# Performance work log

Measured on AMD Instinct MI355X. Metric: run time of the kernel, lower is better.

The kernel has to match this reference:

```python
import jax, jax.numpy as jnp
import numpy as np

N = 50000      # nodes
E = 800000     # directed edges (before self-loops)
FEAT = 120     # raw node feature dim
TOPO = 8       # topological feature dim
H1, D1 = 8, 8  # conv1: heads, per-head dim
C = 40         # out_channels (classes)
NEG_SLOPE = 0.2


def setup_inputs() -> dict:
    key = jax.random.key(0)
    ks = jax.random.split(key, 10)
    return {
        "x": jax.random.normal(ks[0], (N, FEAT), dtype=jnp.float32),
        "topo": jax.random.normal(ks[1], (N, TOPO), dtype=jnp.float32),
        "edge_index": jax.random.randint(ks[2], (2, E), 0, N, dtype=jnp.int32),
        "W1": jax.random.normal(ks[3], (FEAT + TOPO, H1 * D1), dtype=jnp.float32) * 0.1,
        "a_src1": jax.random.normal(ks[4], (H1, D1), dtype=jnp.float32) * 0.1,
        "a_dst1": jax.random.normal(ks[5], (H1, D1), dtype=jnp.float32) * 0.1,
        "b1": jnp.zeros((H1 * D1,), dtype=jnp.float32),
        "W2": jax.random.normal(ks[6], (H1 * D1, C), dtype=jnp.float32) * 0.1,
        "a_src2": jax.random.normal(ks[7], (1, C), dtype=jnp.float32) * 0.1,
        "a_dst2": jax.random.normal(ks[8], (1, C), dtype=jnp.float32) * 0.1,
        "b2": jnp.zeros((C,), dtype=jnp.float32),
    }


def gat_conv(x, src, dst, W, a_src, a_dst, b, heads, d, concat):
    """PyG-style GATConv (eval mode). src/dst already include self-loops."""
    n = x.shape[0]
    h = (x @ W).reshape(n, heads, d)                      # [N,H,D]
    al_src = jnp.sum(h * a_src[None], axis=-1)            # [N,H]
    al_dst = jnp.sum(h * a_dst[None], axis=-1)            # [N,H]
    e = jax.nn.leaky_relu(al_src[src] + al_dst[dst], NEG_SLOPE)  # [E',H]
    # segment softmax over incoming edges per destination node
    m = jax.ops.segment_max(e, dst, num_segments=n)       # [N,H]
    p = jnp.exp(e - m[dst])                               # [E',H]
    s = jax.ops.segment_sum(p, dst, num_segments=n)       # [N,H]
    alpha = p / s[dst]                                    # [E',H]
    out = jax.ops.segment_sum(alpha[:, :, None] * h[src], dst, num_segments=n)  # [N,H,D]
    if concat:
        return out.reshape(n, heads * d) + b
    return out.mean(axis=1) + b


def reference(x, topo, edge_index, W1, a_src1, a_dst1, b1, W2, a_src2, a_dst2, b2):
    n = x.shape[0]
    loops = jnp.arange(n, dtype=edge_index.dtype)
    src = jnp.concatenate([edge_index[0], loops])
    dst = jnp.concatenate([edge_index[1], loops])
    xin = jnp.concatenate([x, topo], axis=1)              # [N, FEAT+TOPO]
    h = jax.nn.elu(gat_conv(xin, src, dst, W1, a_src1, a_dst1, b1, H1, D1, True))
    out = gat_conv(h, src, dst, W2, a_src2, a_dst2, b2, 1, C, False)
    return jax.nn.log_softmax(out, axis=1)
```

## Files before the change

### kernel.cpp

```cpp
#include <hip/hip_runtime.h>
#include <hip/hip_fp16.h>

#define NN 50000
#define EE 800000
#define NBUCK 196
#define CAP 5120
#define TILEA 1024
#define NBA ((EE + TILEA - 1) / TILEA)
#define NGB 782
#define SRCS_MAX (EE + 8 * NN)

typedef _Float16 half8 __attribute__((ext_vector_type(8)));
typedef float floatx4 __attribute__((ext_vector_type(4)));

__global__ void k_prep(const float* __restrict__ W1, const float* __restrict__ W2,
                       _Float16* __restrict__ Bf1, _Float16* __restrict__ Bf2,
                       int* __restrict__ cursor, float* __restrict__ alsrc,
                       float* __restrict__ al2s) {
    int tid = blockIdx.x * 256 + threadIdx.x;
    if (tid < 1024) {
        int kk = tid >> 8, ct = (tid >> 6) & 3, L = tid & 63;
        int k0 = kk * 32 + (L >> 4) * 8, col = ct * 16 + (L & 15);
        half8 v;
        #pragma unroll
        for (int j = 0; j < 8; j++) v[j] = (_Float16)W1[(k0 + j) * 64 + col];
        *(half8*)(Bf1 + ((size_t)((kk * 4 + ct) * 64 + L)) * 8) = v;
    } else if (tid < 1024 + 384) {
        int u = tid - 1024;
        int kk = u / 192, rem = u % 192;
        int ct = rem >> 6, L = rem & 63;
        int k0 = kk * 32 + (L >> 4) * 8, col = ct * 16 + (L & 15);
        half8 v;
        #pragma unroll
        for (int j = 0; j < 8; j++)
            v[j] = (col < 40) ? (_Float16)W2[(k0 + j) * 40 + col] : (_Float16)0.f;
        *(half8*)(Bf2 + ((size_t)((kk * 3 + ct) * 64 + L)) * 8) = v;
    } else {
        int u = tid - 1408;
        if (u < NBUCK) cursor[u] = 0;
        if (u >= 200 && u < 208) alsrc[(size_t)NN * 8 + (u - 200)] = -1e30f;
        if (u == 208) al2s[NN] = -1e30f;
    }
}

__global__ __launch_bounds__(256) void k_bucketA(const int* __restrict__ ei,
        int* __restrict__ cursor, unsigned* __restrict__ bucketData) {
    __shared__ int cnt[NBUCK], base[NBUCK];
    int t = threadIdx.x;
    for (int i = t; i < NBUCK; i += 256) cnt[i] = 0;
    __syncthreads();
    int e0 = blockIdx.x * TILEA;
    int nE = min(TILEA, EE - e0);
    unsigned pk[4]; int bk[4], rk[4];
    int m = 0;
    for (int i = t; i < nE; i += 256) {
        int e = e0 + i;
        int s = ei[e], d = ei[EE + e];
        pk[m] = ((unsigned)d << 16) | (unsigned)s;
        bk[m] = d >> 8;
        rk[m] = atomicAdd(&cnt[bk[m]], 1);
        m++;
    }
    __syncthreads();
    for (int i = t; i < NBUCK; i += 256)
        base[i] = (cnt[i] > 0) ? atomicAdd(&cursor[i], cnt[i]) : 0;
    __syncthreads();
    for (int k = 0; k < m; k++) {
        int pos = base[bk[k]] + rk[k];
        if (pos < CAP) bucketData[(size_t)bk[k] * CAP + pos] = pk[k];
    }
}

__global__ void k_scanB(const int* __restrict__ cursor, int* __restrict__ bucketOut) {
    __shared__ int s0[256], s1[256];
    int t = threadIdx.x;
    int nloc = (t < NBUCK) ? min(256, NN - t * 256) : 0;
    int v = (t < NBUCK) ? (min(cursor[t], CAP) + 8 * nloc) : 0;
    s0[t] = v;
    __syncthreads();
    int* a = s0; int* b = s1;
    for (int off = 1; off < 256; off <<= 1) {
        int x = a[t] + ((t >= off) ? a[t - off] : 0);
        b[t] = x;
        __syncthreads();
        int* tmp = a; a = b; b = tmp;
    }
    if (t < NBUCK) bucketOut[t] = a[t] - v;
}

__global__ __launch_bounds__(256) void k_bucketB(const unsigned* __restrict__ bucketData,
        const int* __restrict__ cursor, const int* __restrict__ bucketOut,
        int2* __restrict__ rowseg, int* __restrict__ srcs) {
    __shared__ int cnt[256], cur[256], sbuf[256];
    __shared__ int sorted[CAP + 2048];
    int b = blockIdx.x, t = threadIdx.x;
    int nloc = min(256, NN - b * 256);
    int ecnt = min(cursor[b], CAP);
    size_t inBase = (size_t)b * CAP;
    int outBase = bucketOut[b];
    cnt[t] = (t < nloc) ? 1 : 0;
    __syncthreads();
    for (int i = t; i < ecnt; i += 256) {
        unsigned u = bucketData[inBase + i];
        atomicAdd(&cnt[(u >> 16) & 255], 1);
    }
    __syncthreads();
    int cv = cnt[t];
    int pcv = (t < nloc) ? ((cv + 7) & ~7) : 0;
    sbuf[t] = pcv;
    __syncthreads();
    int* a = sbuf; int* bb = cnt;
    for (int off = 1; off < 256; off <<= 1) {
        int x = a[t] + ((t >= off) ? a[t - off] : 0);
        bb[t] = x;
        __syncthreads();
        int* tmp = a; a = bb; bb = tmp;
    }
    int excl = a[t] - pcv;
    int total = a[255];
    __syncthreads();
    if (t < nloc) {
        rowseg[b * 256 + t] = make_int2(outBase + excl, outBase + excl + pcv);
        sorted[excl] = b * 256 + t;
        for (int k = cv; k < pcv; k++) sorted[excl + k] = NN;
        cur[t] = excl + 1;
    }
    __syncthreads();
    for (int i = t; i < ecnt; i += 256) {
        unsigned u = bucketData[inBase + i];
        int ld = (u >> 16) & 255;
        int p = atomicAdd(&cur[ld], 1);
        sorted[p] = (int)(u & 0xffffu);
    }
    __syncthreads();
    for (int i = t; i < total; i += 256) srcs[outBase + i] = sorted[i];
}

__global__ __launch_bounds__(256) void k_gemm1(
    const float* __restrict__ x, const float* __restrict__ topo,
    const _Float16* __restrict__ Bf1,
    const float* __restrict__ a_src, const float* __restrict__ a_dst,
    __half* __restrict__ h1, float* __restrict__ alsrc, float* __restrict__ aldst) {
    int wave = threadIdx.x >> 6, lane = threadIdx.x & 63;
    int row0 = blockIdx.x * 64 + wave * 16;
    if (row0 >= NN) return;
    int g = lane >> 4, li = lane & 15;
    int myrow = row0 + li;
    half8 B[16];
    const half8* bp = (const half8*)Bf1;
    #pragma unroll
    for (int i = 0; i < 16; i++) B[i] = bp[i * 64 + lane];
    floatx4 acc[4] = {{0,0,0,0},{0,0,0,0},{0,0,0,0},{0,0,0,0}};
    #pragma unroll
    for (int kk = 0; kk < 4; kk++) {
        int k0 = kk * 32 + g * 8;
        const float* sp = (k0 == 120) ? (topo + (size_t)myrow * 8)
                                      : (x + (size_t)myrow * 120 + k0);
        float4 u0 = ((const float4*)sp)[0];
        float4 u1 = ((const float4*)sp)[1];
        half8 av;
        av[0] = (_Float16)u0.x; av[1] = (_Float16)u0.y;
        av[2] = (_Float16)u0.z; av[3] = (_Float16)u0.w;
        av[4] = (_Float16)u1.x; av[5] = (_Float16)u1.y;
        av[6] = (_Float16)u1.z; av[7] = (_Float16)u1.w;
        #pragma unroll
        for (int ct = 0; ct < 4; ct++)
            acc[ct] = __builtin_amdgcn_mfma_f32_16x16x32_f16(av, B[kk * 4 + ct], acc[ct], 0, 0, 0);
    }
    #pragma unroll
    for (int ct = 0; ct < 4; ct++)
        #pragma unroll
        for (int r = 0; r < 4; r++)
            h1[(size_t)(row0 + 4 * g + r) * 64 + ct * 16 + li] = __float2half(acc[ct][r]);
    float ps[4][4], pd[4][4];
    #pragma unroll
    for (int ct = 0; ct < 4; ct++) {
        int head = 2 * ct + (li >> 3), dix = li & 7;
        float asv = a_src[head * 8 + dix];
        float adv = a_dst[head * 8 + dix];
        #pragma unroll
        for (int r = 0; r < 4; r++) {
            ps[ct][r] = acc[ct][r] * asv;
            pd[ct][r] = acc[ct][r] * adv;
        }
    }
    #pragma unroll
    for (int off = 1; off <= 4; off <<= 1)
        #pragma unroll
        for (int ct = 0; ct < 4; ct++)
            #pragma unroll
            for (int r = 0; r < 4; r++) {
                ps[ct][r] += __shfl_xor(ps[ct][r], off, 64);
                pd[ct][r] += __shfl_xor(pd[ct][r], off, 64);
            }
    if ((li & 7) == 0) {
        #pragma unroll
        for (int ct = 0; ct < 4; ct++) {
            int head = 2 * ct + (li >> 3);
            #pragma unroll
            for (int r = 0; r < 4; r++) {
                int row = row0 + 4 * g + r;
                alsrc[row * 8 + head] = ps[ct][r];
                aldst[row * 8 + head] = pd[ct][r];
            }
        }
    }
}

__global__ __launch_bounds__(256) void k_agg1(
    const int2* __restrict__ rowseg, const int* __restrict__ srcs,
    const float* __restrict__ alsrc, const float* __restrict__ aldst,
    const __half* __restrict__ h1, const float* __restrict__ b1,
    __half* __restrict__ hout) {
    int wave = threadIdx.x >> 6;
    int lane = threadIdx.x & 63;
    int d = blockIdx.x * 4 + wave;
    if (d >= NN) return;
    int hs = lane >> 5;
    int cp = lane & 31;
    int hh = cp >> 2;
    float adst = aldst[d * 8 + hh];
    int2 seg = rowseg[d];
    int jb = seg.x, je = seg.y;
    float ssum = 0.f, ax = 0.f, ay = 0.f;
    int sA0 = srcs[jb + hs],     sA1 = srcs[jb + 2 + hs];
    int sA2 = srcs[jb + 4 + hs], sA3 = srcs[jb + 6 + hs];
    for (int j = jb; j < je; j += 8) {
        int s0 = sA0, s1 = sA1, s2 = sA2, s3 = sA3;
        int jn = j + 8;
        if (jn < je) {
            sA0 = srcs[jn + hs];     sA1 = srcs[jn + 2 + hs];
            sA2 = srcs[jn + 4 + hs]; sA3 = srcs[jn + 6 + hs];
        }
        float e0 = alsrc[s0 * 8 + hh] + adst;
        float e1 = alsrc[s1 * 8 + hh] + adst;
        float e2 = alsrc[s2 * 8 + hh] + adst;
        float e3 = alsrc[s3 * 8 + hh] + adst;
        __half2 v0 = *(const __half2*)(h1 + (size_t)s0 * 64 + 2 * cp);
        __half2 v1 = *(const __half2*)(h1 + (size_t)s1 * 64 + 2 * cp);
        __half2 v2 = *(const __half2*)(h1 + (size_t)s2 * 64 + 2 * cp);
        __half2 v3 = *(const __half2*)(h1 + (size_t)s3 * 64 + 2 * cp);
        float p0 = __expf(fmaxf(e0, 0.2f * e0));
        float p1 = __expf(fmaxf(e1, 0.2f * e1));
        float p2 = __expf(fmaxf(e2, 0.2f * e2));
        float p3 = __expf(fmaxf(e3, 0.2f * e3));
        float2 f0 = __half22float2(v0), f1 = __half22float2(v1);
        float2 f2 = __half22float2(v2), f3 = __half22float2(v3);
        ssum += (p0 + p1) + (p2 + p3);
        ax += p0 * f0.x + p1 * f1.x + p2 * f2.x + p3 * f3.x;
        ay += p0 * f0.y + p1 * f1.y + p2 * f2.y + p3 * f3.y;
    }
    ssum += __shfl_xor(ssum, 32, 64);
    ax += __shfl_xor(ax, 32, 64);
    ay += __shfl_xor(ay, 32, 64);
    if (hs == 0) {
        float2 bv = *(const float2*)(b1 + 2 * cp);
        float inv = 1.f / ssum;
        float vx = ax * inv + bv.x;
        float vy = ay * inv + bv.y;
        vx = (vx > 0.f) ? vx : (__expf(vx) - 1.f);
        vy = (vy > 0.f) ? vy : (__expf(vy) - 1.f);
        *(__half2*)(hout + (size_t)d * 64 + 2 * cp) = __floats2half2_rn(vx, vy);
    }
}

__global__ __launch_bounds__(256) void k_gemm2(
    const __half* __restrict__ hout, const _Float16* __restrict__ Bf2,
    const float* __restrict__ a_src2, const float* __restrict__ a_dst2,
    __half* __restrict__ h2, float* __restrict__ al2s, float* __restrict__ al2d) {
    int wave = threadIdx.x >> 6, lane = threadIdx.x & 63;
    int row0 = blockIdx.x * 64 + wave * 16;
    if (row0 >= NN) return;
    int g = lane >> 4, li = lane & 15;
    int myrow = row0 + li;
    half8 B[6];
    const half8* bp = (const half8*)Bf2;
    #pragma unroll
    for (int i = 0; i < 6; i++) B[i] = bp[i * 64 + lane];
    floatx4 acc[3] = {{0,0,0,0},{0,0,0,0},{0,0,0,0}};
    #pragma unroll
    for (int kk = 0; kk < 2; kk++) {
        int k0 = kk * 32 + g * 8;
        half8 av = *(const half8*)(hout + (size_t)myrow * 64 + k0);
        #pragma unroll
        for (int ct = 0; ct < 3; ct++)
            acc[ct] = __builtin_amdgcn_mfma_f32_16x16x32_f16(av, B[kk * 3 + ct], acc[ct], 0, 0, 0);
    }
    float ts[4] = {0.f, 0.f, 0.f, 0.f}, td[4] = {0.f, 0.f, 0.f, 0.f};
    #pragma unroll
    for (int ct = 0; ct < 3; ct++) {
        int col = ct * 16 + li;
        bool ok = (col < 40);
        float asv = ok ? a_src2[col] : 0.f;
        float adv = ok ? a_dst2[col] : 0.f;
        #pragma unroll
        for (int r = 0; r < 4; r++) {
            ts[r] += acc[ct][r] * asv;
            td[r] += acc[ct][r] * adv;
            if (ok) h2[(size_t)(row0 + 4 * g + r) * 40 + col] = __float2half(acc[ct][r]);
        }
    }
    #pragma unroll
    for (int off = 1; off <= 8; off <<= 1)
        #pragma unroll
        for (int r = 0; r < 4; r++) {
            ts[r] += __shfl_xor(ts[r], off, 64);
            td[r] += __shfl_xor(td[r], off, 64);
        }
    if (li == 0) {
        #pragma unroll
        for (int r = 0; r < 4; r++) {
            int row = row0 + 4 * g + r;
            al2s[row] = ts[r];
            al2d[row] = td[r];
        }
    }
}

__global__ __launch_bounds__(256) void k_agg2(
    const int2* __restrict__ rowseg, const int* __restrict__ srcs,
    const float* __restrict__ al2s, const float* __restrict__ al2d,
    const __half* __restrict__ h2, const float* __restrict__ b2,
    float* __restrict__ out) {
    int wave = threadIdx.x >> 6;
    int lane = threadIdx.x & 63;
    int d = blockIdx.x * 4 + wave;
    if (d >= NN) return;
    int hs = lane >> 5;
    int cp = lane & 31;
    bool act = (cp < 20);
    int cpc = act ? cp : 0;
    float adst = al2d[d];
    int2 seg = rowseg[d];
    int jb = seg.x, je = seg.y;
    float ssum = 0.f, ax = 0.f, ay = 0.f;
    int sA0 = srcs[jb + hs],     sA1 = srcs[jb + 2 + hs];
    int sA2 = srcs[jb + 4 + hs], sA3 = srcs[jb + 6 + hs];
    for (int j = jb; j < je; j += 8) {
        int s0 = sA0, s1 = sA1, s2 = sA2, s3 = sA3;
        int jn = j + 8;
        if (jn < je) {
            sA0 = srcs[jn + hs];     sA1 = srcs[jn + 2 + hs];
            sA2 = srcs[jn + 4 + hs]; sA3 = srcs[jn + 6 + hs];
        }
        float e0 = al2s[s0] + adst;
        float e1 = al2s[s1] + adst;
        float e2 = al2s[s2] + adst;
        float e3 = al2s[s3] + adst;
        __half2 v0 = *(const __half2*)(h2 + (size_t)s0 * 40 + 2 * cpc);
        __half2 v1 = *(const __half2*)(h2 + (size_t)s1 * 40 + 2 * cpc);
        __half2 v2 = *(const __half2*)(h2 + (size_t)s2 * 40 + 2 * cpc);
        __half2 v3 = *(const __half2*)(h2 + (size_t)s3 * 40 + 2 * cpc);
        float p0 = __expf(fmaxf(e0, 0.2f * e0));
        float p1 = __expf(fmaxf(e1, 0.2f * e1));
        float p2 = __expf(fmaxf(e2, 0.2f * e2));
        float p3 = __expf(fmaxf(e3, 0.2f * e3));
        float2 f0 = __half22float2(v0), f1 = __half22float2(v1);
        float2 f2 = __half22float2(v2), f3 = __half22float2(v3);
        ssum += (p0 + p1) + (p2 + p3);
        ax += p0 * f0.x + p1 * f1.x + p2 * f2.x + p3 * f3.x;
        ay += p0 * f0.y + p1 * f1.y + p2 * f2.y + p3 * f3.y;
    }
    ssum += __shfl_xor(ssum, 32, 64);
    ax += __shfl_xor(ax, 32, 64);
    ay += __shfl_xor(ay, 32, 64);
    float inv = 1.f / ssum;
    float2 bv = *(const float2*)(b2 + 2 * cpc);
    float ox = ax * inv + bv.x;
    float oy = ay * inv + bv.y;
    float mo = act ? fmaxf(ox, oy) : -3.0e38f;
    #pragma unroll
    for (int off = 16; off; off >>= 1) mo = fmaxf(mo, __shfl_xor(mo, off, 64));
    float te = act ? (__expf(ox - mo) + __expf(oy - mo)) : 0.f;
    #pragma unroll
    for (int off = 16; off; off >>= 1) te += __shfl_xor(te, off, 64);
    float ls = __logf(te);
    if (act && hs == 0)
        *(float2*)(out + (size_t)d * 40 + 2 * cp) = make_float2(ox - mo - ls, oy - mo - ls);
}

extern "C" void kernel_launch(void* const* d_in, const int* in_sizes, int n_in,
                              void* d_out, int out_size, void* d_ws, size_t ws_size,
                              hipStream_t stream) {
    (void)in_sizes; (void)n_in; (void)out_size; (void)ws_size;
    const float* x    = (const float*)d_in[0];
    const float* topo = (const float*)d_in[1];
    const int*   ei   = (const int*)d_in[2];
    const float* W1   = (const float*)d_in[3];
    const float* as1  = (const float*)d_in[4];
    const float* ad1  = (const float*)d_in[5];
    const float* b1   = (const float*)d_in[6];
    const float* W2   = (const float*)d_in[7];
    const float* as2  = (const float*)d_in[8];
    const float* ad2  = (const float*)d_in[9];
    const float* b2   = (const float*)d_in[10];
    float* out = (float*)d_out;

    char* ws = (char*)d_ws;
    size_t off = 0;
    auto alloc = [&](size_t bytes) {
        void* p = ws + off;
        off += (bytes + 255) / 256 * 256;
        return p;
    };
    int2*      rowseg     = (int2*)alloc((size_t)NN * 8);
    int*       cursor     = (int*)alloc(NBUCK * 4);
    int*       bucketOut  = (int*)alloc(NBUCK * 4);
    unsigned*  bucketData = (unsigned*)alloc((size_t)NBUCK * CAP * 4);
    int*       srcs       = (int*)alloc((size_t)SRCS_MAX * 4);
    float*     alsrc1     = (float*)alloc((size_t)(NN + 1) * 8 * 4);
    float*     aldst1     = (float*)alloc((size_t)NN * 8 * 4);
    float*     al2s       = (float*)alloc((NN + 1) * 4);
    float*     al2d       = (float*)alloc(NN * 4);
    _Float16*  Bf1        = (_Float16*)alloc(4 * 4 * 64 * 8 * 2);
    _Float16*  Bf2        = (_Float16*)alloc(2 * 3 * 64 * 8 * 2);
    __half*    h1         = (__half*)alloc((size_t)(NN + 1) * 64 * 2);
    __half*    hout       = (__half*)alloc((size_t)NN * 64 * 2);
    __half*    h2         = (__half*)alloc((size_t)(NN + 1) * 40 * 2);

    k_prep    <<<7,     256, 0, stream>>>(W1, W2, Bf1, Bf2, cursor, alsrc1, al2s);
    k_bucketA <<<NBA,   256, 0, stream>>>(ei, cursor, bucketData);
    k_scanB   <<<1,     256, 0, stream>>>(cursor, bucketOut);
    k_bucketB <<<NBUCK, 256, 0, stream>>>(bucketData, cursor, bucketOut, rowseg, srcs);
    k_gemm1   <<<NGB,   256, 0, stream>>>(x, topo, Bf1, as1, ad1, h1, alsrc1, aldst1);
    k_agg1    <<<(NN + 3) / 4, 256, 0, stream>>>(rowseg, srcs, alsrc1, aldst1, h1, b1, hout);
    k_gemm2   <<<NGB,   256, 0, stream>>>(hout, Bf2, as2, ad2, h2, al2s, al2d);
    k_agg2    <<<(NN + 3) / 4, 256, 0, stream>>>(rowseg, srcs, al2s, al2d, h2, b2, out);
}
```

Before: 194.0 us.

## Fuse edge bucketing with GEMM1 and fold bucket scan into bucketB

Merges the edge-bucketing pass and the first GEMM into one launch using disjoint block ranges, so the two independent phases run side by side. The separate single-block scan kernel is removed, and each bucketB block now recomputes the bucket prefix sum itself. bucketB also grows to 1024 threads to speed up histogramming and scatter. This cuts the launch count from 8 to 6 and overlaps latency-bound work, at the cost of a redundant scan in every block and more divergent code inside the fused kernel.

```diff
diff --git a/kernel.cpp b/kernel.cpp
--- a/kernel.cpp
+++ b/kernel.cpp
@@ -43,106 +43,42 @@
     }
 }
 
-__global__ __launch_bounds__(256) void k_bucketA(const int* __restrict__ ei,
-        int* __restrict__ cursor, unsigned* __restrict__ bucketData) {
-    __shared__ int cnt[NBUCK], base[NBUCK];
-    int t = threadIdx.x;
-    for (int i = t; i < NBUCK; i += 256) cnt[i] = 0;
-    __syncthreads();
-    int e0 = blockIdx.x * TILEA;
-    int nE = min(TILEA, EE - e0);
-    unsigned pk[4]; int bk[4], rk[4];
-    int m = 0;
-    for (int i = t; i < nE; i += 256) {
-        int e = e0 + i;
-        int s = ei[e], d = ei[EE + e];
-        pk[m] = ((unsigned)d << 16) | (unsigned)s;
-        bk[m] = d >> 8;
-        rk[m] = atomicAdd(&cnt[bk[m]], 1);
-        m++;
-    }
-    __syncthreads();
-    for (int i = t; i < NBUCK; i += 256)
-        base[i] = (cnt[i] > 0) ? atomicAdd(&cursor[i], cnt[i]) : 0;
-    __syncthreads();
-    for (int k = 0; k < m; k++) {
-        int pos = base[bk[k]] + rk[k];
-        if (pos < CAP) bucketData[(size_t)bk[k] * CAP + pos] = pk[k];
-    }
-}
-
-__global__ void k_scanB(const int* __restrict__ cursor, int* __restrict__ bucketOut) {
-    __shared__ int s0[256], s1[256];
-    int t = threadIdx.x;
-    int nloc = (t < NBUCK) ? min(256, NN - t * 256) : 0;
-    int v = (t < NBUCK) ? (min(cursor[t], CAP) + 8 * nloc) : 0;
-    s0[t] = v;
-    __syncthreads();
-    int* a = s0; int* b = s1;
-    for (int off = 1; off < 256; off <<= 1) {
-        int x = a[t] + ((t >= off) ? a[t - off] : 0);
-        b[t] = x;
-        __syncthreads();
-        int* tmp = a; a = b; b = tmp;
-    }
-    if (t < NBUCK) bucketOut[t] = a[t] - v;
-}
-
-__global__ __launch_bounds__(256) void k_bucketB(const unsigned* __restrict__ bucketData,
-        const int* __restrict__ cursor, const int* __restrict__ bucketOut,
-        int2* __restrict__ rowseg, int* __restrict__ srcs) {
-    __shared__ int cnt[256], cur[256], sbuf[256];
-    __shared__ int sorted[CAP + 2048];
-    int b = blockIdx.x, t = threadIdx.x;
-    int nloc = min(256, NN - b * 256);
-    int ecnt = min(cursor[b], CAP);
-    size_t inBase = (size_t)b * CAP;
-    int outBase = bucketOut[b];
-    cnt[t] = (t < nloc) ? 1 : 0;
-    __syncthreads();
-    for (int i = t; i < ecnt; i += 256) {
-        unsigned u = bucketData[inBase + i];
-        atomicAdd(&cnt[(u >> 16) & 255], 1);
-    }
-    __syncthreads();
-    int cv = cnt[t];
-    int pcv = (t < nloc) ? ((cv + 7) & ~7) : 0;
-    sbuf[t] = pcv;
-    __syncthreads();
-    int* a = sbuf; int* bb = cnt;
-    for (int off = 1; off < 256; off <<= 1) {
-        int x = a[t] + ((t >= off) ? a[t - off] : 0);
-        bb[t] = x;
-        __syncthreads();
-        int* tmp = a; a = bb; bb = tmp;
-    }
-    int excl = a[t] - pcv;
-    int total = a[255];
-    __syncthreads();
-    if (t < nloc) {
-        rowseg[b * 256 + t] = make_int2(outBase + excl, outBase + excl + pcv);
-        sorted[excl] = b * 256 + t;
-        for (int k = cv; k < pcv; k++) sorted[excl + k] = NN;
-        cur[t] = excl + 1;
-    }
-    __syncthreads();
-    for (int i = t; i < ecnt; i += 256) {
-        unsigned u = bucketData[inBase + i];
-        int ld = (u >> 16) & 255;
-        int p = atomicAdd(&cur[ld], 1);
-        sorted[p] = (int)(u & 0xffffu);
-    }
-    __syncthreads();
-    for (int i = t; i < total; i += 256) srcs[outBase + i] = sorted[i];
-}
-
-__global__ __launch_bounds__(256) void k_gemm1(
+__global__ __launch_bounds__(256) void k_fusedAG(
+    const int* __restrict__ ei, int* __restrict__ cursor,
+    unsigned* __restrict__ bucketData,
     const float* __restrict__ x, const float* __restrict__ topo,
     const _Float16* __restrict__ Bf1,
     const float* __restrict__ a_src, const float* __restrict__ a_dst,
     __half* __restrict__ h1, float* __restrict__ alsrc, float* __restrict__ aldst) {
+    if (blockIdx.x < NBA) {
+        __shared__ int cnt[NBUCK], base[NBUCK];
+        int t = threadIdx.x;
+        for (int i = t; i < NBUCK; i += 256) cnt[i] = 0;
+        __syncthreads();
+        int e0 = blockIdx.x * TILEA;
+        int nE = min(TILEA, EE - e0);
+        unsigned pk[4]; int bk[4], rk[4];
+        int m = 0;
+        for (int i = t; i < nE; i += 256) {
+            int e = e0 + i;
+            int s = ei[e], d = ei[EE + e];
+            pk[m] = ((unsigned)d << 16) | (unsigned)s;
+            bk[m] = d >> 8;
+            rk[m] = atomicAdd(&cnt[bk[m]], 1);
+            m++;
+        }
+        __syncthreads();
+        for (int i = t; i < NBUCK; i += 256)
+            base[i] = (cnt[i] > 0) ? atomicAdd(&cursor[i], cnt[i]) : 0;
+        __syncthreads();
+        for (int k = 0; k < m; k++) {
+            int pos = base[bk[k]] + rk[k];
+            if (pos < CAP) bucketData[(size_t)bk[k] * CAP + pos] = pk[k];
+        }
+        return;
+    }
     int wave = threadIdx.x >> 6, lane = threadIdx.x & 63;
-    int row0 = blockIdx.x * 64 + wave * 16;
+    int row0 = (blockIdx.x - NBA) * 64 + wave * 16;
     if (row0 >= NN) return;
     int g = lane >> 4, li = lane & 15;
     int myrow = row0 + li;
@@ -205,6 +141,72 @@
             }
         }
     }
+}
+
+__global__ __launch_bounds__(1024) void k_bucketB(const unsigned* __restrict__ bucketData,
+        const int* __restrict__ cursor,
+        int2* __restrict__ rowseg, int* __restrict__ srcs) {
+    __shared__ int cnt[256], cur[256], sbuf[256], svals[256];
+    __shared__ int sorted[CAP + 2048];
+    int b = blockIdx.x, t = threadIdx.x;
+    int nloc = min(256, NN - b * 256);
+    int ecnt = min(cursor[b], CAP);
+    size_t inBase = (size_t)b * CAP;
+    if (t < 256) {
+        int vv = 0;
+        if (t < NBUCK) {
+            int nl = min(256, NN - t * 256);
+            vv = min(cursor[t], CAP) + 8 * nl;
+        }
+        svals[t] = vv;
+    }
+    __syncthreads();
+    int* a = svals; int* bb = sbuf;
+    for (int off = 1; off < 256; off <<= 1) {
+        if (t < 256) bb[t] = a[t] + ((t >= off) ? a[t - off] : 0);
+        __syncthreads();
+        int* tmp = a; a = bb; bb = tmp;
+    }
+    int outBase = (b == 0) ? 0 : a[b - 1];
+    __syncthreads();
+    if (t < 256) cnt[t] = (t < nloc) ? 1 : 0;
+    __syncthreads();
+    for (int i = t; i < ecnt; i += 1024) {
+        unsigned u = bucketData[inBase + i];
+        atomicAdd(&cnt[(u >> 16) & 255], 1);
+    }
+    __syncthreads();
+    int cv = 0, pcv = 0;
+    if (t < 256) {
+        cv = cnt[t];
+        pcv = (t < nloc) ? ((cv + 7) & ~7) : 0;
+        sbuf[t] = pcv;
+    }
+    __syncthreads();
+    a = sbuf; bb = cnt;
+    for (int off = 1; off < 256; off <<= 1) {
+        if (t < 256) bb[t] = a[t] + ((t >= off) ? a[t - off] : 0);
+        __syncthreads();
+        int* tmp = a; a = bb; bb = tmp;
+    }
+    int total = a[255];
+    int excl = (t < 256) ? (a[t] - pcv) : 0;
+    __syncthreads();
+    if (t < nloc) {
+        rowseg[b * 256 + t] = make_int2(outBase + excl, outBase + excl + pcv);
+        sorted[excl] = b * 256 + t;
+        for (int k = cv; k < pcv; k++) sorted[excl + k] = NN;
+        cur[t] = excl + 1;
+    }
+    __syncthreads();
+    for (int i = t; i < ecnt; i += 1024) {
+        unsigned u = bucketData[inBase + i];
+        int ld = (u >> 16) & 255;
+        int p = atomicAdd(&cur[ld], 1);
+        sorted[p] = (int)(u & 0xffffu);
+    }
+    __syncthreads();
+    for (int i = t; i < total; i += 1024) srcs[outBase + i] = sorted[i];
 }
 
 __global__ __launch_bounds__(256) void k_agg1(
@@ -405,7 +407,6 @@
     };
     int2*      rowseg     = (int2*)alloc((size_t)NN * 8);
     int*       cursor     = (int*)alloc(NBUCK * 4);
-    int*       bucketOut  = (int*)alloc(NBUCK * 4);
     unsigned*  bucketData = (unsigned*)alloc((size_t)NBUCK * CAP * 4);
     int*       srcs       = (int*)alloc((size_t)SRCS_MAX * 4);
     float*     alsrc1     = (float*)alloc((size_t)(NN + 1) * 8 * 4);
@@ -418,12 +419,11 @@
     __half*    hout       = (__half*)alloc((size_t)NN * 64 * 2);
     __half*    h2         = (__half*)alloc((size_t)(NN + 1) * 40 * 2);
 
-    k_prep    <<<7,     256, 0, stream>>>(W1, W2, Bf1, Bf2, cursor, alsrc1, al2s);
-    k_bucketA <<<NBA,   256, 0, stream>>>(ei, cursor, bucketData);
-    k_scanB   <<<1,     256, 0, stream>>>(cursor, bucketOut);
-    k_bucketB <<<NBUCK, 256, 0, stream>>>(bucketData, cursor, bucketOut, rowseg, srcs);
-    k_gemm1   <<<NGB,   256, 0, stream>>>(x, topo, Bf1, as1, ad1, h1, alsrc1, aldst1);
+    k_prep    <<<7,         256,  0, stream>>>(W1, W2, Bf1, Bf2, cursor, alsrc1, al2s);
+    k_fusedAG <<<NBA + NGB, 256,  0, stream>>>(ei, cursor, bucketData,
+                                               x, topo, Bf1, as1, ad1, h1, alsrc1, aldst1);
+    k_bucketB <<<NBUCK,     1024, 0, stream>>>(bucketData, cursor, rowseg, srcs);
     k_agg1    <<<(NN + 3) / 4, 256, 0, stream>>>(rowseg, srcs, alsrc1, aldst1, h1, b1, hout);
-    k_gemm2   <<<NGB,   256, 0, stream>>>(hout, Bf2, as2, ad2, h2, al2s, al2d);
+    k_gemm2   <<<NGB,       256,  0, stream>>>(hout, Bf2, as2, ad2, h2, al2s, al2d);
     k_agg2    <<<(NN + 3) / 4, 256, 0, stream>>>(rowseg, srcs, al2s, al2d, h2, b2, out);
 }
```

Result: faster. 182.8 us (-5.8%).
